# Optimization experiments

Hardware: AMD Instinct MI355X
Metric: run time of the kernel (lower is better)

## Reference

```python
import jax, jax.numpy as jnp
import numpy as np


def _leaf_exps(inc, depth):
    # inc: (B, N, d). Restricted tensor exponential of each increment:
    # level k = inc^{tensor k} / k!, stored flat as (B, N, d**k).
    levels = [inc]
    for k in range(2, depth + 1):
        prev = levels[-1]  # (B, N, d**(k-1))
        nxt = (prev[..., :, None] * inc[..., None, :]).reshape(prev.shape[0], prev.shape[1], -1) / k
        levels.append(nxt)
    return levels


def _chen_mult(a, b):
    # Truncated tensor-algebra product (Chen's relation), flat levels.
    # C_k = A_k + B_k + sum_{i=1}^{k-1} A_i (x) B_{k-i}
    depth = len(a)
    out = []
    for k in range(1, depth + 1):
        c = a[k - 1] + b[k - 1]
        for i in range(1, k):
            c = c + (a[i - 1][..., :, None] * b[k - i - 1][..., None, :]).reshape(c.shape)
        out.append(c)
    return out


def _signature(path, depth):
    # path: (B, L, d) -> tuple of levels (B, d), (B, d^2), ..., (B, d^depth)
    inc = path[:, 1:] - path[:, :-1]  # (B, L-1, d)
    B, n, d = inc.shape
    N = 1 << (n - 1).bit_length()  # next power of 2 (static)
    if N != n:
        # zero increment -> identity element of the truncated tensor algebra
        inc = jnp.pad(inc, ((0, 0), (0, N - n), (0, 0)))
    levels = _leaf_exps(inc, depth)
    # log2(N) rounds of pairwise Chen multiplication (binary tree reduction)
    while levels[0].shape[1] > 1:
        a = [lv[:, 0::2] for lv in levels]
        b = [lv[:, 1::2] for lv in levels]
        levels = _chen_mult(a, b)
    return tuple(lv[:, 0] for lv in levels)


def setup_inputs() -> dict:
    key = jax.random.key(0)
    path = jax.random.normal(key, (32, 1024, 8), dtype=jnp.float32) * 0.1
    return {"path": path, "depth": 4}


def reference(path, depth):
    return _signature(path, depth)
```

## Files before the change

### kernel.cpp

```cpp
#include <hip/hip_runtime.h>


#define D 8
#define LPATH 1024
#define BATCH 32
#define NCHUNK 8
#define MSTEP 128
#define SIG_STRIDE 4680
#define OFF2 8
#define OFF3 72
#define OFF4 584
#define N13F4 146

__device__ __forceinline__ void load8(const float* __restrict__ p, float* dst) {
  float4 lo = *(const float4*)p;
  float4 hi = *(const float4*)(p + 4);
  dst[0] = lo.x; dst[1] = lo.y; dst[2] = lo.z; dst[3] = lo.w;
  dst[4] = hi.x; dst[5] = hi.y; dst[6] = hi.z; dst[7] = hi.w;
}

__device__ __forceinline__ void store8(float* __restrict__ p, const float* src) {
  *(float4*)p       = make_float4(src[0], src[1], src[2], src[3]);
  *(float4*)(p + 4) = make_float4(src[4], src[5], src[6], src[7]);
}

__global__ __launch_bounds__(256) void sig_chunk128(const float* __restrict__ path,
                                                    float* __restrict__ ws) {
  __shared__ alignas(16) float lp[129 * D];

  const int tid  = threadIdx.x;
  const int lane = tid & 63;
  const int q    = tid >> 6;
  const int b = blockIdx.x >> 3;
  const int c = blockIdx.x & (NCHUNK - 1);
  const int i = lane >> 3;
  const int j = lane & 7;
  const int k0 = q * 2;

  const int g0 = c * MSTEP;
  const int nrows = (129 < LPATH - g0) ? 129 : (LPATH - g0);
  const int nf4 = nrows * 2;
  const float* __restrict__ bp = path + (size_t)b * (LPATH * D) + (size_t)g0 * D;

#pragma unroll
  for (int it = 0; it < 2; ++it) {
    int n = tid + it * 256;
    if (n < nf4) *(float4*)&lp[4 * n] = *(const float4*)(bp + 4 * n);
  }
  __syncthreads();

  float cm[D];
  *(float4*)&cm[0] = *(const float4*)&lp[0];
  *(float4*)&cm[4] = *(const float4*)&lp[4];
  float cwi = lp[i], cwj = lp[j];

  float s1 = 0.f, s2 = 0.f;
  float s3[D] = {0.f, 0.f, 0.f, 0.f, 0.f, 0.f, 0.f, 0.f};
  float s4[2][D];
#pragma unroll
  for (int t = 0; t < 2; ++t)
#pragma unroll
    for (int m = 0; m < D; ++m) s4[t][m] = 0.f;

#pragma unroll 1
  for (int t = 0; t < MSTEP; ++t) {
    int rc = t + 1;
    rc = rc < nrows ? rc : nrows - 1;
    float nm[D];
    *(float4*)&nm[0] = *(const float4*)&lp[rc * D];
    *(float4*)&nm[4] = *(const float4*)&lp[rc * D + 4];
    float nwi = lp[rc * D + i];
    float nwj = lp[rc * D + j];

    float wm[D];
#pragma unroll
    for (int m = 0; m < D; ++m) wm[m] = nm[m] - cm[m];
    float wi = nwi - cwi, wj = nwj - cwj;

    float h1  = __builtin_fmaf(wi, 0.25f, s1);
    float h2  = __builtin_fmaf(h1, wj * (1.f / 3.f), s2);
    float hb2 = h2 * 0.5f;
    float b3a = __builtin_fmaf(hb2, wm[k0], s3[k0]);
    float b3b = __builtin_fmaf(hb2, wm[k0 + 1], s3[k0 + 1]);
#pragma unroll
    for (int m = 0; m < D; ++m) s4[0][m] = __builtin_fmaf(b3a, wm[m], s4[0][m]);
#pragma unroll
    for (int m = 0; m < D; ++m) s4[1][m] = __builtin_fmaf(b3b, wm[m], s4[1][m]);

    float c1 = __builtin_fmaf(wi, (1.f / 3.f), s1);
    float c2 = __builtin_fmaf(c1, wj * 0.5f, s2);
#pragma unroll
    for (int k = 0; k < D; ++k) s3[k] = __builtin_fmaf(c2, wm[k], s3[k]);

    float d1 = __builtin_fmaf(wi, 0.5f, s1);
    s2 = __builtin_fmaf(d1, wj, s2);
    s1 += wi;

#pragma unroll
    for (int m = 0; m < D; ++m) cm[m] = nm[m];
    cwi = nwi; cwj = nwj;
  }

  float* __restrict__ slot = ws + (size_t)(b * NCHUNK + c) * SIG_STRIDE;
  store8(slot + OFF4 + lane * 64 + k0 * 8, s4[0]);
  store8(slot + OFF4 + lane * 64 + (k0 + 1) * 8, s4[1]);
  if (q == 0) {
    if (j == 0) slot[i] = s1;
    slot[OFF2 + lane] = s2;
    store8(slot + OFF3 + lane * 8, s3);
  }
}

__device__ __forceinline__ void fold_lds(const float* __restrict__ L,
                                         const float b4[2][D], float& s1,
                                         float& s2, float s3[D], float s4[2][D],
                                         int i, int j, int lane, int k0) {
  float b1i = L[i];
  float b1j = L[j];
  float sb1[D];
#pragma unroll
  for (int m = 0; m < D; ++m) sb1[m] = L[m];
  float b2own = L[OFF2 + lane];
  float b2row[D], b3own[D];
  *(float4*)&b2row[0] = *(const float4*)&L[OFF2 + j * 8];
  *(float4*)&b2row[4] = *(const float4*)&L[OFF2 + j * 8 + 4];
  *(float4*)&b3own[0] = *(const float4*)&L[OFF3 + lane * 8];
  *(float4*)&b3own[4] = *(const float4*)&L[OFF3 + lane * 8 + 4];

#pragma unroll
  for (int t = 0; t < 2; ++t) {
    const int k = k0 + t;
    float b2k[D], b3k[D];
    *(float4*)&b2k[0] = *(const float4*)&L[OFF2 + k * 8];
    *(float4*)&b2k[4] = *(const float4*)&L[OFF2 + k * 8 + 4];
    *(float4*)&b3k[0] = *(const float4*)&L[OFF3 + (j * 8 + k) * 8];
    *(float4*)&b3k[4] = *(const float4*)&L[OFF3 + (j * 8 + k) * 8 + 4];
    float a3k = s3[k];
#pragma unroll
    for (int m = 0; m < D; ++m) {
      float v = __builtin_fmaf(a3k, sb1[m], s4[t][m] + b4[t][m]);
      v = __builtin_fmaf(s2, b2k[m], v);
      s4[t][m] = __builtin_fmaf(s1, b3k[m], v);
    }
  }
#pragma unroll
  for (int k = 0; k < D; ++k) {
    float v = __builtin_fmaf(s1, b2row[k], s3[k] + b3own[k]);
    s3[k] = __builtin_fmaf(s2, sb1[k], v);
  }
  s2 = s2 + b2own + s1 * b1j;
  s1 = s1 + b1i;
}

__device__ __forceinline__ void staged_folds(const float* __restrict__ base,
                                             int nsig, float (*lds13)[592],
                                             int tid, int i, int j, int lane,
                                             int k0, float& s1, float& s2,
                                             float s3[D], float s4[2][D]) {
  s1 = base[i];
  s2 = base[OFF2 + lane];
  load8(base + OFF3 + lane * 8, s3);
  load8(base + OFF4 + lane * 64 + k0 * 8, s4[0]);
  load8(base + OFF4 + lane * 64 + (k0 + 1) * 8, s4[1]);

  const float* __restrict__ B1p = base + (size_t)SIG_STRIDE;
  float b4cur[2][D];
  load8(B1p + OFF4 + lane * 64 + k0 * 8, b4cur[0]);
  load8(B1p + OFF4 + lane * 64 + (k0 + 1) * 8, b4cur[1]);
  if (tid < N13F4) {
    float4 sv = *(const float4*)(B1p + tid * 4);
    *(float4*)&lds13[1][tid * 4] = sv;
  }
  __syncthreads();

#pragma unroll 1
  for (int c = 1; c < nsig; ++c) {
    const bool more = (c + 1 < nsig);
    const float* __restrict__ Bn = base + (size_t)(c + 1) * SIG_STRIDE;
    float4 svn;
    float b4n[2][D];
    if (more) {
      if (tid < N13F4) svn = *(const float4*)(Bn + tid * 4);
      load8(Bn + OFF4 + lane * 64 + k0 * 8, b4n[0]);
      load8(Bn + OFF4 + lane * 64 + (k0 + 1) * 8, b4n[1]);
    }

    fold_lds(lds13[c & 1], b4cur, s1, s2, s3, s4, i, j, lane, k0);

    if (more) {
      if (tid < N13F4) *(float4*)&lds13[(c + 1) & 1][tid * 4] = svn;
#pragma unroll
      for (int t = 0; t < 2; ++t)
#pragma unroll
        for (int m = 0; m < D; ++m) b4cur[t][m] = b4n[t][m];
    }
    __syncthreads();
  }
}

__global__ __launch_bounds__(256) void sig_fold8f(const float* __restrict__ ws,
                                                  float* __restrict__ out) {
  __shared__ alignas(16) float lds13[2][592];
  const int tid  = threadIdx.x;
  const int q    = tid >> 6;
  const int lane = tid & 63;
  const int bb = blockIdx.x;
  const int i = lane >> 3;
  const int j = lane & 7;
  const int k0 = q * 2;

  const float* __restrict__ base = ws + (size_t)bb * NCHUNK * SIG_STRIDE;

  float s1, s2, s3[D], s4[2][D];
  staged_folds(base, NCHUNK, lds13, tid, i, j, lane, k0, s1, s2, s3, s4);

  if (q == 0) {
    if (j == 0) out[bb * 8 + i] = s1;
    out[256 + bb * 64 + lane] = s2;
    store8(out + 2304 + bb * 512 + lane * 8, s3);
  }
  store8(out + 18688 + bb * 4096 + lane * 64 + k0 * 8, s4[0]);
  store8(out + 18688 + bb * 4096 + lane * 64 + (k0 + 1) * 8, s4[1]);
}

extern "C" void kernel_launch(void* const* d_in, const int* in_sizes, int n_in,
                              void* d_out, int out_size, void* d_ws, size_t ws_size,
                              hipStream_t stream) {
  const float* path = (const float*)d_in[0];
  float* out = (float*)d_out;
  float* ws  = (float*)d_ws;

  sig_chunk128<<<dim3(256), dim3(256), 0, stream>>>(path, ws);
  sig_fold8f<<<dim3(BATCH), dim3(256), 0, stream>>>(ws, out);
}
```

Baseline: 92.83 us.

## Precompute increments in LDS and split level-3 state across wavefronts

The chunk kernel now computes path increments once while staging into shared memory, so the sequential loop reads increments directly instead of differencing consecutive rows each step. Level-3 accumulators are split so each of the four wavefronts keeps only its two k entries rather than all eight redundantly, and the same split carries into the fold kernel and the output stores. The inner loop is unrolled by four. This cuts redundant per-step arithmetic and registers, in exchange for a different LDS layout and more unrolled code size.

```diff
diff --git a/kernel.cpp b/kernel.cpp
--- a/kernel.cpp
+++ b/kernel.cpp
@@ -26,7 +26,7 @@
 
 __global__ __launch_bounds__(256) void sig_chunk128(const float* __restrict__ path,
                                                     float* __restrict__ ws) {
-  __shared__ alignas(16) float lp[129 * D];
+  __shared__ alignas(16) float wl[MSTEP * D];
 
   const int tid  = threadIdx.x;
   const int lane = tid & 63;
@@ -39,49 +39,42 @@
 
   const int g0 = c * MSTEP;
   const int nrows = (129 < LPATH - g0) ? 129 : (LPATH - g0);
-  const int nf4 = nrows * 2;
   const float* __restrict__ bp = path + (size_t)b * (LPATH * D) + (size_t)g0 * D;
 
-#pragma unroll
-  for (int it = 0; it < 2; ++it) {
-    int n = tid + it * 256;
-    if (n < nf4) *(float4*)&lp[4 * n] = *(const float4*)(bp + 4 * n);
+  {
+    const int n = tid;
+    const int t = n >> 1;
+    float4 w = make_float4(0.f, 0.f, 0.f, 0.f);
+    if (t < nrows - 1) {
+      float4 a0 = *(const float4*)(bp + 4 * n);
+      float4 a1 = *(const float4*)(bp + 4 * n + D);
+      w = make_float4(a1.x - a0.x, a1.y - a0.y, a1.z - a0.z, a1.w - a0.w);
+    }
+    *(float4*)&wl[4 * n] = w;
   }
   __syncthreads();
 
-  float cm[D];
-  *(float4*)&cm[0] = *(const float4*)&lp[0];
-  *(float4*)&cm[4] = *(const float4*)&lp[4];
-  float cwi = lp[i], cwj = lp[j];
-
-  float s1 = 0.f, s2 = 0.f;
-  float s3[D] = {0.f, 0.f, 0.f, 0.f, 0.f, 0.f, 0.f, 0.f};
+  float s1 = 0.f, s2 = 0.f, s3a = 0.f, s3b = 0.f;
   float s4[2][D];
 #pragma unroll
   for (int t = 0; t < 2; ++t)
 #pragma unroll
     for (int m = 0; m < D; ++m) s4[t][m] = 0.f;
 
-#pragma unroll 1
+#pragma unroll 4
   for (int t = 0; t < MSTEP; ++t) {
-    int rc = t + 1;
-    rc = rc < nrows ? rc : nrows - 1;
-    float nm[D];
-    *(float4*)&nm[0] = *(const float4*)&lp[rc * D];
-    *(float4*)&nm[4] = *(const float4*)&lp[rc * D + 4];
-    float nwi = lp[rc * D + i];
-    float nwj = lp[rc * D + j];
-
     float wm[D];
-#pragma unroll
-    for (int m = 0; m < D; ++m) wm[m] = nm[m] - cm[m];
-    float wi = nwi - cwi, wj = nwj - cwj;
+    *(float4*)&wm[0] = *(const float4*)&wl[t * D];
+    *(float4*)&wm[4] = *(const float4*)&wl[t * D + 4];
+    const float wi = wl[t * D + i];
+    const float wj = wl[t * D + j];
+    const float2 wk = *(const float2*)&wl[t * D + k0];
 
     float h1  = __builtin_fmaf(wi, 0.25f, s1);
     float h2  = __builtin_fmaf(h1, wj * (1.f / 3.f), s2);
     float hb2 = h2 * 0.5f;
-    float b3a = __builtin_fmaf(hb2, wm[k0], s3[k0]);
-    float b3b = __builtin_fmaf(hb2, wm[k0 + 1], s3[k0 + 1]);
+    float b3a = __builtin_fmaf(hb2, wk.x, s3a);
+    float b3b = __builtin_fmaf(hb2, wk.y, s3b);
 #pragma unroll
     for (int m = 0; m < D; ++m) s4[0][m] = __builtin_fmaf(b3a, wm[m], s4[0][m]);
 #pragma unroll
@@ -89,43 +82,38 @@
 
     float c1 = __builtin_fmaf(wi, (1.f / 3.f), s1);
     float c2 = __builtin_fmaf(c1, wj * 0.5f, s2);
-#pragma unroll
-    for (int k = 0; k < D; ++k) s3[k] = __builtin_fmaf(c2, wm[k], s3[k]);
+    s3a = __builtin_fmaf(c2, wk.x, s3a);
+    s3b = __builtin_fmaf(c2, wk.y, s3b);
 
     float d1 = __builtin_fmaf(wi, 0.5f, s1);
     s2 = __builtin_fmaf(d1, wj, s2);
     s1 += wi;
-
-#pragma unroll
-    for (int m = 0; m < D; ++m) cm[m] = nm[m];
-    cwi = nwi; cwj = nwj;
   }
 
   float* __restrict__ slot = ws + (size_t)(b * NCHUNK + c) * SIG_STRIDE;
   store8(slot + OFF4 + lane * 64 + k0 * 8, s4[0]);
   store8(slot + OFF4 + lane * 64 + (k0 + 1) * 8, s4[1]);
+  *(float2*)(slot + OFF3 + lane * 8 + k0) = make_float2(s3a, s3b);
   if (q == 0) {
     if (j == 0) slot[i] = s1;
     slot[OFF2 + lane] = s2;
-    store8(slot + OFF3 + lane * 8, s3);
   }
 }
 
 __device__ __forceinline__ void fold_lds(const float* __restrict__ L,
                                          const float b4[2][D], float& s1,
-                                         float& s2, float s3[D], float s4[2][D],
-                                         int i, int j, int lane, int k0) {
+                                         float& s2, float& s3a, float& s3b,
+                                         float s4[2][D], int i, int j, int lane,
+                                         int k0) {
   float b1i = L[i];
   float b1j = L[j];
   float sb1[D];
 #pragma unroll
   for (int m = 0; m < D; ++m) sb1[m] = L[m];
+  const float2 sb1k = *(const float2*)&L[k0];
   float b2own = L[OFF2 + lane];
-  float b2row[D], b3own[D];
-  *(float4*)&b2row[0] = *(const float4*)&L[OFF2 + j * 8];
-  *(float4*)&b2row[4] = *(const float4*)&L[OFF2 + j * 8 + 4];
-  *(float4*)&b3own[0] = *(const float4*)&L[OFF3 + lane * 8];
-  *(float4*)&b3own[4] = *(const float4*)&L[OFF3 + lane * 8 + 4];
+  const float2 b2rj = *(const float2*)&L[OFF2 + j * 8 + k0];
+  const float2 b3oj = *(const float2*)&L[OFF3 + lane * 8 + k0];
 
 #pragma unroll
   for (int t = 0; t < 2; ++t) {
@@ -135,7 +123,7 @@
     *(float4*)&b2k[4] = *(const float4*)&L[OFF2 + k * 8 + 4];
     *(float4*)&b3k[0] = *(const float4*)&L[OFF3 + (j * 8 + k) * 8];
     *(float4*)&b3k[4] = *(const float4*)&L[OFF3 + (j * 8 + k) * 8 + 4];
-    float a3k = s3[k];
+    const float a3k = (t == 0) ? s3a : s3b;
 #pragma unroll
     for (int m = 0; m < D; ++m) {
       float v = __builtin_fmaf(a3k, sb1[m], s4[t][m] + b4[t][m]);
@@ -143,11 +131,8 @@
       s4[t][m] = __builtin_fmaf(s1, b3k[m], v);
     }
   }
-#pragma unroll
-  for (int k = 0; k < D; ++k) {
-    float v = __builtin_fmaf(s1, b2row[k], s3[k] + b3own[k]);
-    s3[k] = __builtin_fmaf(s2, sb1[k], v);
-  }
+  s3a = __builtin_fmaf(s2, sb1k.x, __builtin_fmaf(s1, b2rj.x, s3a + b3oj.x));
+  s3b = __builtin_fmaf(s2, sb1k.y, __builtin_fmaf(s1, b2rj.y, s3b + b3oj.y));
   s2 = s2 + b2own + s1 * b1j;
   s1 = s1 + b1i;
 }
@@ -156,10 +141,12 @@
                                              int nsig, float (*lds13)[592],
                                              int tid, int i, int j, int lane,
                                              int k0, float& s1, float& s2,
-                                             float s3[D], float s4[2][D]) {
+                                             float& s3a, float& s3b,
+                                             float s4[2][D]) {
   s1 = base[i];
   s2 = base[OFF2 + lane];
-  load8(base + OFF3 + lane * 8, s3);
+  const float2 s3i = *(const float2*)(base + OFF3 + lane * 8 + k0);
+  s3a = s3i.x; s3b = s3i.y;
   load8(base + OFF4 + lane * 64 + k0 * 8, s4[0]);
   load8(base + OFF4 + lane * 64 + (k0 + 1) * 8, s4[1]);
 
@@ -185,7 +172,7 @@
       load8(Bn + OFF4 + lane * 64 + (k0 + 1) * 8, b4n[1]);
     }
 
-    fold_lds(lds13[c & 1], b4cur, s1, s2, s3, s4, i, j, lane, k0);
+    fold_lds(lds13[c & 1], b4cur, s1, s2, s3a, s3b, s4, i, j, lane, k0);
 
     if (more) {
       if (tid < N13F4) *(float4*)&lds13[(c + 1) & 1][tid * 4] = svn;
@@ -211,14 +198,14 @@
 
   const float* __restrict__ base = ws + (size_t)bb * NCHUNK * SIG_STRIDE;
 
-  float s1, s2, s3[D], s4[2][D];
-  staged_folds(base, NCHUNK, lds13, tid, i, j, lane, k0, s1, s2, s3, s4);
+  float s1, s2, s3a, s3b, s4[2][D];
+  staged_folds(base, NCHUNK, lds13, tid, i, j, lane, k0, s1, s2, s3a, s3b, s4);
 
   if (q == 0) {
     if (j == 0) out[bb * 8 + i] = s1;
     out[256 + bb * 64 + lane] = s2;
-    store8(out + 2304 + bb * 512 + lane * 8, s3);
-  }
+  }
+  *(float2*)(out + 2304 + bb * 512 + lane * 8 + k0) = make_float2(s3a, s3b);
   store8(out + 18688 + bb * 4096 + lane * 64 + k0 * 8, s4[0]);
   store8(out + 18688 + bb * 4096 + lane * 64 + (k0 + 1) * 8, s4[1]);
 }
```

Result: faster. 74.66 us (median of 2 runs) (-19.6%).
